# Kernel optimization log

Hardware: AMD Instinct MI355X
Metric: run time of the kernel (lower is better)

Reference implementation:

```python
import jax, jax.numpy as jnp
import numpy as np

WS = 7        # window_size
SHIFT = 3     # shift_size
NH = 3        # num_heads
E = 96        # embed_dim
B, H, W = 8, 224, 224


def _relative_position_index(ws: int) -> np.ndarray:
    coords = np.stack(np.meshgrid(np.arange(ws), np.arange(ws), indexing='ij')).reshape(2, -1)
    rel = coords[:, :, None] - coords[:, None, :]          # (2, N, N)
    rel = rel.transpose(1, 2, 0) + (ws - 1)                # (N, N, 2)
    rel[:, :, 0] *= 2 * ws - 1
    return rel.sum(-1)                                      # (N, N) in [0, (2ws-1)^2)


def setup_inputs() -> dict:
    key = jax.random.key(0)
    ks = jax.random.split(key, 6)
    x = jax.random.normal(ks[0], (B, H, W, E), dtype=jnp.float32)
    # nn.MultiheadAttention params: packed in_proj (3E,E)+(3E,), out_proj (E,E)+(E,)
    w_qkv = jax.random.normal(ks[1], (3 * E, E), dtype=jnp.float32) * 0.02
    b_qkv = jax.random.normal(ks[2], (3 * E,), dtype=jnp.float32) * 0.02
    w_out = jax.random.normal(ks[3], (E, E), dtype=jnp.float32) * 0.02
    b_out = jax.random.normal(ks[4], (E,), dtype=jnp.float32) * 0.02
    bias_table = jax.random.normal(ks[5], ((2 * WS - 1) ** 2, NH), dtype=jnp.float32) * 0.02
    rel_index = jnp.asarray(_relative_position_index(WS), dtype=jnp.int32)
    return {"x": x, "w_qkv": w_qkv, "b_qkv": b_qkv, "w_out": w_out,
            "b_out": b_out, "bias_table": bias_table, "rel_index": rel_index}


def reference(x, w_qkv, b_qkv, w_out, b_out, bias_table, rel_index):
    ws, shift = WS, SHIFT
    Bq, Hq, Wq, C = x.shape
    nh = bias_table.shape[-1]
    hd = C // nh
    N = ws * ws

    # cyclic shift
    xs = jnp.roll(x, (-shift, -shift), axis=(1, 2))

    Hp = -(-Hq // ws) * ws
    Wp = -(-Wq // ws) * ws
    xs = jnp.pad(xs, ((0, 0), (0, Hp - Hq), (0, Wp - Wq), (0, 0)))

    # window partition -> (B*nW, N, C)
    win = xs.reshape(Bq, Hp // ws, ws, Wp // ws, ws, C)
    win = win.transpose(0, 1, 3, 2, 4, 5).reshape(-1, N, C)

    # packed QKV projection (torch Linear: x @ W.T + b)
    qkv = win @ w_qkv.T + b_qkv
    q, k, v = jnp.split(qkv, 3, axis=-1)
    hsplit = lambda t: t.reshape(t.shape[0], N, nh, hd)
    q, k, v = hsplit(q), hsplit(k), hsplit(v)

    # scaled attention scores + relative position bias (used as attn_mask in torch)
    scale = 1.0 / jnp.sqrt(jnp.asarray(hd, dtype=q.dtype))
    scores = jnp.einsum('bnhd,bmhd->bhnm', q * scale, k)    # (B*nW, h, N, N)
    bias = bias_table[rel_index].transpose(2, 0, 1)         # (h, N, N)
    attn = jax.nn.softmax(scores + bias[None], axis=-1)

    out = jnp.einsum('bhnm,bmhd->bnhd', attn, v).reshape(-1, N, C)
    out = out @ w_out.T + b_out

    # window reverse + crop + reverse shift
    out = out.reshape(Bq, Hp // ws, Wp // ws, ws, ws, C)
    out = out.transpose(0, 1, 3, 2, 4, 5).reshape(Bq, Hp, Wp, C)[:, :Hq, :Wq, :]
    return jnp.roll(out, (shift, shift), axis=(1, 2))
```

## Files before the change

### kernel.cpp

```cpp
#include <hip/hip_runtime.h>
#include <cstddef>


typedef _Float16 half8 __attribute__((ext_vector_type(8)));
typedef float f4v __attribute__((ext_vector_type(4)));
typedef unsigned short u16;
typedef unsigned int u32;

#define MFMA(A, B, C) __builtin_amdgcn_mfma_f32_16x16x32_f16((A), (B), (C), 0, 0, 0)

__device__ inline u16 f16b(float f) { return __builtin_bit_cast(u16, (_Float16)f); }
__device__ inline u32 pkrtz(float a, float b) {
    return __builtin_bit_cast(u32, __builtin_amdgcn_cvt_pkrtz(a, b));
}
__device__ inline int SWU(int a, int kg) {
    return (((a ^ (kg << 1) ^ ((a & 8) >> 1)) & 15) | (kg << 4));
}

__global__ void prep_kernel(const float* __restrict__ wqkv, const float* __restrict__ wout,
                            const float* __restrict__ btab, const int* __restrict__ ridx,
                            const float* __restrict__ bqkv,
                            u16* __restrict__ wq16, u16* __restrict__ wo16,
                            float* __restrict__ bmat, float* __restrict__ bqs)
{
    const int i = blockIdx.x * 256 + threadIdx.x;
    const float QS = 0.17677669529663688f * 1.4426950408889634f;
    if (i < 27648) {
        float f = wqkv[i];
        if (i < 9216) f *= QS;
        wq16[i] = f16b(f);
    } else if (i < 36864) {
        wo16[i - 27648] = f16b(wout[i - 27648]);
    } else if (i < 49152) {
        const int j = i - 36864;
        const int h = j >> 12, rem = j & 4095, r = rem >> 6, u = rem & 63;
        bmat[j] = (r < 49 && u < 49) ? btab[ridx[r * 49 + u] * 3 + h] * 1.4426950408889634f : 0.f;
    } else if (i < 49440) {
        const int j = i - 49152;
        float f = bqkv[j];
        if (j < 96) f *= QS;
        bqs[j] = f;
    }
}

__global__ __launch_bounds__(256, 4)
void swin_kernel(const float* __restrict__ x,
                 const u16* __restrict__ wq16,
                 const u16* __restrict__ wo16,
                 const float* __restrict__ bqs,
                 const float* __restrict__ bout,
                 const float* __restrict__ bm,
                 float* __restrict__ out)
{
    __shared__ __attribute__((aligned(16))) char smem[40960];
    constexpr int QT = 0, KT = 12288, VT = 24576, PL = 36864;

    const int tid  = threadIdx.x;
    const int w    = tid >> 6;
    const int lane = tid & 63;
    const int l15  = lane & 15;
    const int lg   = lane >> 4;

    const int blk = blockIdx.x;
    const int bb  = blk >> 10;
    const int wi7 = ((blk >> 5) & 31) * 7;
    const int wj7 = (blk & 31) * 7;

    const int swbase = SWU(l15, lg) * 16;
    const int elb    = ((lg & 1) * 4) * 2;

    half8 xb[4][3];
    #pragma unroll
    for (int m = 0; m < 4; ++m) {
        const int t = m * 16 + l15;
        const int tr = t / 7, tc = t - tr * 7;
        int r = wi7 + tr + 3; if (r >= 224) r -= 224;
        int c = wj7 + tc + 3; if (c >= 224) c -= 224;
        const float* xrow = x + ((size_t)((bb * 224 + r) * 224 + c)) * 96 + lg * 8;
        #pragma unroll
        for (int ks = 0; ks < 3; ++ks) {
            const float4 f0 = *(const float4*)(xrow + ks * 32);
            const float4 f1 = *(const float4*)(xrow + ks * 32 + 4);
            uint4 pk;
            pk.x = pkrtz(f0.x, f0.y); pk.y = pkrtz(f0.z, f0.w);
            pk.z = pkrtz(f1.x, f1.y); pk.w = pkrtz(f1.z, f1.w);
            xb[m][ks] = __builtin_bit_cast(half8, pk);
        }
    }
    {
        const u16* wbase = wq16 + (size_t)l15 * 96 + lg * 8;
        half8 bcur[3], bnxt[3];
        int n = w;
        {
            const u16* p = wbase + n * 1536;
            bcur[0] = *(const half8*)(p);
            bcur[1] = *(const half8*)(p + 32);
            bcur[2] = *(const half8*)(p + 64);
        }
        while (true) {
            const int n2 = n + 4;
            if (n2 < 18) {
                const u16* p = wbase + n2 * 1536;
                bnxt[0] = *(const half8*)(p);
                bnxt[1] = *(const half8*)(p + 32);
                bnxt[2] = *(const half8*)(p + 64);
            }
            if (n < 12) {
                const float4 b4 = *(const float4*)(bqs + n * 16 + lg * 4);
                const int kg = ((n & 1) << 1) + (lg >> 1);
                const int fr0 = (n < 6) ? (QT + (((n >> 1) * 4) << 10))
                                        : (KT + ((((n - 6) >> 1) * 4) << 10));
                #pragma unroll
                for (int m = 0; m < 4; ++m) {
                    f4v acc = {0.f, 0.f, 0.f, 0.f};
                    acc = MFMA(bcur[0], xb[m][0], acc);
                    acc = MFMA(bcur[1], xb[m][1], acc);
                    acc = MFMA(bcur[2], xb[m][2], acc);
                    uint2 pv;
                    pv.x = pkrtz(acc[0] + b4.x, acc[1] + b4.y);
                    pv.y = pkrtz(acc[2] + b4.z, acc[3] + b4.w);
                    *(uint2*)(smem + fr0 + (m << 10) + SWU(l15, kg) * 16 + elb) = pv;
                }
            } else {
                const float bv = bqs[n * 16 + l15];
                const int hh = (n - 12) >> 1, nd = n & 1;
                const int fr0 = VT + (((hh * 2 + nd) * 2) << 10);
                #pragma unroll
                for (int m = 0; m < 4; ++m) {
                    f4v acc = {0.f, 0.f, 0.f, 0.f};
                    acc = MFMA(xb[m][0], bcur[0], acc);
                    acc = MFMA(xb[m][1], bcur[1], acc);
                    acc = MFMA(xb[m][2], bcur[2], acc);
                    uint2 pv;
                    pv.x = pkrtz(acc[0] + bv, acc[1] + bv);
                    pv.y = pkrtz(acc[2] + bv, acc[3] + bv);
                    const int kg = ((m & 1) << 1) + (lg >> 1);
                    *(uint2*)(smem + fr0 + ((m >> 1) << 10) + SWU(l15, kg) * 16 + elb) = pv;
                }
            }
            if (n2 >= 18) break;
            bcur[0] = bnxt[0]; bcur[1] = bnxt[1]; bcur[2] = bnxt[2];
            n = n2;
        }
    }
    __syncthreads();

    {
        const int t = w * 16 + l15;
        half8 qa = *(const half8*)(smem + QT + ((0 * 4 + w) << 10) + swbase);
        half8 kb[4];
        #pragma unroll
        for (int ut = 0; ut < 4; ++ut)
            kb[ut] = *(const half8*)(smem + KT + ((0 * 4 + ut) << 10) + swbase);

        #pragma unroll
        for (int h = 0; h < 3; ++h) {
            const int qfr = QT + ((h * 4 + w) << 10);
            f4v s[4];
            #pragma unroll
            for (int ut = 0; ut < 4; ++ut) {
                f4v z = {0.f, 0.f, 0.f, 0.f};
                s[ut] = MFMA(kb[ut], qa, z);
            }
            half8 qan; half8 kbn[4];
            if (h < 2) {
                qan = *(const half8*)(smem + QT + (((h + 1) * 4 + w) << 10) + swbase);
                #pragma unroll
                for (int ut = 0; ut < 4; ++ut)
                    kbn[ut] = *(const half8*)(smem + KT + (((h + 1) * 4 + ut) << 10) + swbase);
            }
            const float* bp = bm + h * 4096 + t * 64 + lg * 4;
            #pragma unroll
            for (int ut = 0; ut < 4; ++ut) {
                const float4 bv = *(const float4*)(bp + ut * 16);
                s[ut][0] += bv.x; s[ut][1] += bv.y; s[ut][2] += bv.z; s[ut][3] += bv.w;
            }
            s[3][1] = -1e30f; s[3][2] = -1e30f; s[3][3] = -1e30f;
            if (lg) s[3][0] = -1e30f;
            float mx = -1e30f;
            #pragma unroll
            for (int ut = 0; ut < 4; ++ut)
                #pragma unroll
                for (int i = 0; i < 4; ++i) mx = fmaxf(mx, s[ut][i]);
            mx = fmaxf(mx, __shfl_xor(mx, 16));
            mx = fmaxf(mx, __shfl_xor(mx, 32));
            float sm = 0.f;
            #pragma unroll
            for (int ut = 0; ut < 4; ++ut)
                #pragma unroll
                for (int i = 0; i < 4; ++i) {
                    const float e = exp2f(s[ut][i] - mx);
                    s[ut][i] = e; sm += e;
                }
            sm += __shfl_xor(sm, 16);
            sm += __shfl_xor(sm, 32);
            const float inv = 1.f / sm;
            #pragma unroll
            for (int ut = 0; ut < 4; ++ut) {
                uint2 pv;
                pv.x = pkrtz(s[ut][0] * inv, s[ut][1] * inv);
                pv.y = pkrtz(s[ut][2] * inv, s[ut][3] * inv);
                const int kg = (ut & 1) * 2 + (lg >> 1);
                const int base = (ut < 2) ? qfr : (PL + (w << 10));
                *(uint2*)(smem + base + SWU(l15, kg) * 16 + elb) = pv;
            }
            const half8 p0 = *(const half8*)(smem + qfr + swbase);
            const half8 p1 = *(const half8*)(smem + PL + (w << 10) + swbase);
            #pragma unroll
            for (int nd = 0; nd < 2; ++nd) {
                f4v o = {0.f, 0.f, 0.f, 0.f};
                o = MFMA(*(const half8*)(smem + VT + (((h * 2 + nd) * 2 + 0) << 10) + swbase), p0, o);
                o = MFMA(*(const half8*)(smem + VT + (((h * 2 + nd) * 2 + 1) << 10) + swbase), p1, o);
                uint2 ov;
                ov.x = pkrtz(o[0], o[1]);
                ov.y = pkrtz(o[2], o[3]);
                const int kg = nd * 2 + (lg >> 1);
                *(uint2*)(smem + qfr + SWU(l15, kg) * 16 + elb) = ov;
            }
            if (h < 2) {
                qa = qan;
                #pragma unroll
                for (int ut = 0; ut < 4; ++ut) kb[ut] = kbn[ut];
            }
        }
    }
    __syncthreads();

    {
        #pragma unroll
        for (int q = 0; q < 6; ++q) {
            const int p = w * 6 + q;
            const int nn = p >> 2, m = p & 3;
            f4v acc = {0.f, 0.f, 0.f, 0.f};
            #pragma unroll
            for (int ks = 0; ks < 3; ++ks) {
                const half8 wa = *(const half8*)(wo16 + (size_t)(nn * 16 + l15) * 96 + ks * 32 + lg * 8);
                const half8 ob = *(const half8*)(smem + QT + ((ks * 4 + m) << 10) + swbase);
                acc = MFMA(wa, ob, acc);
            }
            const int t = m * 16 + l15;
            if (t < 49) {
                const int tr = t / 7, tc = t - tr * 7;
                int r = wi7 + tr + 3; if (r >= 224) r -= 224;
                int c = wj7 + tc + 3; if (c >= 224) c -= 224;
                const float4 bo = *(const float4*)(bout + nn * 16 + lg * 4);
                float4 res;
                res.x = acc[0] + bo.x; res.y = acc[1] + bo.y;
                res.z = acc[2] + bo.z; res.w = acc[3] + bo.w;
                *(float4*)(out + ((size_t)((bb * 224 + r) * 224 + c)) * 96 + nn * 16 + lg * 4) = res;
            }
        }
    }
}

extern "C" void kernel_launch(void* const* d_in, const int* in_sizes, int n_in,
                              void* d_out, int out_size, void* d_ws, size_t ws_size,
                              hipStream_t stream) {
    const float* x          = (const float*)d_in[0];
    const float* w_qkv      = (const float*)d_in[1];
    const float* b_qkv      = (const float*)d_in[2];
    const float* w_out      = (const float*)d_in[3];
    const float* b_out      = (const float*)d_in[4];
    const float* bias_table = (const float*)d_in[5];
    const int*   rel_index  = (const int*)d_in[6];
    float* outp = (float*)d_out;

    u16* wq16 = (u16*)d_ws;
    u16* wo16 = wq16 + 27648;
    float* bmat = (float*)((char*)d_ws + 73728);
    float* bqs  = (float*)((char*)d_ws + 122880);

    prep_kernel<<<dim3(194), dim3(256), 0, stream>>>(
        w_qkv, w_out, bias_table, rel_index, b_qkv, wq16, wo16, bmat, bqs);
    swin_kernel<<<dim3(8192), dim3(256), 0, stream>>>(
        x, wq16, wo16, bqs, b_out, bmat, outp);
}
```

Before: 219.2 us.

## Pre-fragment bias with mask, software-pipeline heads, drop barrier before out-projection

The bias matrix is now stored in MFMA fragment order with -inf padding baked in, so it can seed the score MFMA accumulator directly. This removes the per-head bias add and the masking writes. The score MFMAs for the next head are issued during the current head's softmax and PV stage, which overlaps the MFMA and VALU work. The out-projection is remapped so each wave uses only its own query rows from shared memory, which lets the final __syncthreads be dropped; the cost is more live registers for the double-buffered scores.

```diff
diff --git a/kernel.cpp b/kernel.cpp
--- a/kernel.cpp
+++ b/kernel.cpp
@@ -21,10 +21,11 @@
                             const float* __restrict__ btab, const int* __restrict__ ridx,
                             const float* __restrict__ bqkv,
                             u16* __restrict__ wq16, u16* __restrict__ wo16,
-                            float* __restrict__ bmat, float* __restrict__ bqs)
+                            float* __restrict__ bmf, float* __restrict__ bqs)
 {
     const int i = blockIdx.x * 256 + threadIdx.x;
-    const float QS = 0.17677669529663688f * 1.4426950408889634f;
+    const float LOG2E = 1.4426950408889634f;
+    const float QS = 0.17677669529663688f * LOG2E;
     if (i < 27648) {
         float f = wqkv[i];
         if (i < 9216) f *= QS;
@@ -32,9 +33,16 @@
     } else if (i < 36864) {
         wo16[i - 27648] = f16b(wout[i - 27648]);
     } else if (i < 49152) {
-        const int j = i - 36864;
-        const int h = j >> 12, rem = j & 4095, r = rem >> 6, u = rem & 63;
-        bmat[j] = (r < 49 && u < 49) ? btab[ridx[r * 49 + u] * 3 + h] * 1.4426950408889634f : 0.f;
+        const int j  = i - 36864;
+        const int fi = j & 3, ln = (j >> 2) & 63, fw = (j >> 8) & 3;
+        const int fut = (j >> 10) & 3, fh = j >> 12;
+        const int u  = fut * 16 + (ln >> 4) * 4 + fi;
+        const int tt = fw * 16 + (ln & 15);
+        float v;
+        if (u >= 49)      v = -1e30f;
+        else if (tt >= 49) v = 0.f;
+        else               v = btab[ridx[tt * 49 + u] * 3 + fh] * LOG2E;
+        bmf[j] = v;
     } else if (i < 49440) {
         const int j = i - 49152;
         float f = bqkv[j];
@@ -49,7 +57,7 @@
                  const u16* __restrict__ wo16,
                  const float* __restrict__ bqs,
                  const float* __restrict__ bout,
-                 const float* __restrict__ bm,
+                 const float* __restrict__ bmf,
                  float* __restrict__ out)
 {
     __shared__ __attribute__((aligned(16))) char smem[40960];
@@ -146,42 +154,44 @@
     __syncthreads();
 
     {
-        const int t = w * 16 + l15;
-        half8 qa = *(const half8*)(smem + QT + ((0 * 4 + w) << 10) + swbase);
-        half8 kb[4];
+        const int plb = PL + (w << 10);
+        half8 qaC, qaN;
+        half8 kb[2][4];
+        f4v   s[2][4];
+        f4v   bC[4];
+
+        qaC = *(const half8*)(smem + QT + ((0 * 4 + w) << 10) + swbase);
         #pragma unroll
         for (int ut = 0; ut < 4; ++ut)
-            kb[ut] = *(const half8*)(smem + KT + ((0 * 4 + ut) << 10) + swbase);
+            kb[0][ut] = *(const half8*)(smem + KT + ((0 * 4 + ut) << 10) + swbase);
+        {
+            const float* bb0 = bmf + w * 256 + lane * 4;
+            #pragma unroll
+            for (int ut = 0; ut < 4; ++ut) bC[ut] = *(const f4v*)(bb0 + ut * 1024);
+        }
+        #pragma unroll
+        for (int ut = 0; ut < 4; ++ut)
+            s[0][ut] = MFMA(kb[0][ut], qaC, bC[ut]);
 
         #pragma unroll
         for (int h = 0; h < 3; ++h) {
+            const int cur = h & 1, nxt = cur ^ 1;
             const int qfr = QT + ((h * 4 + w) << 10);
-            f4v s[4];
-            #pragma unroll
-            for (int ut = 0; ut < 4; ++ut) {
-                f4v z = {0.f, 0.f, 0.f, 0.f};
-                s[ut] = MFMA(kb[ut], qa, z);
-            }
-            half8 qan; half8 kbn[4];
             if (h < 2) {
-                qan = *(const half8*)(smem + QT + (((h + 1) * 4 + w) << 10) + swbase);
+                qaN = *(const half8*)(smem + QT + (((h + 1) * 4 + w) << 10) + swbase);
                 #pragma unroll
                 for (int ut = 0; ut < 4; ++ut)
-                    kbn[ut] = *(const half8*)(smem + KT + (((h + 1) * 4 + ut) << 10) + swbase);
-            }
-            const float* bp = bm + h * 4096 + t * 64 + lg * 4;
-            #pragma unroll
-            for (int ut = 0; ut < 4; ++ut) {
-                const float4 bv = *(const float4*)(bp + ut * 16);
-                s[ut][0] += bv.x; s[ut][1] += bv.y; s[ut][2] += bv.z; s[ut][3] += bv.w;
-            }
-            s[3][1] = -1e30f; s[3][2] = -1e30f; s[3][3] = -1e30f;
-            if (lg) s[3][0] = -1e30f;
-            float mx = -1e30f;
-            #pragma unroll
-            for (int ut = 0; ut < 4; ++ut)
-                #pragma unroll
-                for (int i = 0; i < 4; ++i) mx = fmaxf(mx, s[ut][i]);
+                    kb[nxt][ut] = *(const half8*)(smem + KT + (((h + 1) * 4 + ut) << 10) + swbase);
+                const float* bbn = bmf + (h + 1) * 4096 + w * 256 + lane * 4;
+                #pragma unroll
+                for (int ut = 0; ut < 4; ++ut) bC[ut] = *(const f4v*)(bbn + ut * 1024);
+            }
+            float mx = fmaxf(fmaxf(s[cur][0][0], s[cur][0][1]), fmaxf(s[cur][0][2], s[cur][0][3]));
+            #pragma unroll
+            for (int ut = 1; ut < 4; ++ut) {
+                mx = fmaxf(mx, fmaxf(fmaxf(s[cur][ut][0], s[cur][ut][1]),
+                                     fmaxf(s[cur][ut][2], s[cur][ut][3])));
+            }
             mx = fmaxf(mx, __shfl_xor(mx, 16));
             mx = fmaxf(mx, __shfl_xor(mx, 32));
             float sm = 0.f;
@@ -189,8 +199,8 @@
             for (int ut = 0; ut < 4; ++ut)
                 #pragma unroll
                 for (int i = 0; i < 4; ++i) {
-                    const float e = exp2f(s[ut][i] - mx);
-                    s[ut][i] = e; sm += e;
+                    const float e = exp2f(s[cur][ut][i] - mx);
+                    s[cur][ut][i] = e; sm += e;
                 }
             sm += __shfl_xor(sm, 16);
             sm += __shfl_xor(sm, 32);
@@ -198,56 +208,61 @@
             #pragma unroll
             for (int ut = 0; ut < 4; ++ut) {
                 uint2 pv;
-                pv.x = pkrtz(s[ut][0] * inv, s[ut][1] * inv);
-                pv.y = pkrtz(s[ut][2] * inv, s[ut][3] * inv);
+                pv.x = pkrtz(s[cur][ut][0] * inv, s[cur][ut][1] * inv);
+                pv.y = pkrtz(s[cur][ut][2] * inv, s[cur][ut][3] * inv);
                 const int kg = (ut & 1) * 2 + (lg >> 1);
-                const int base = (ut < 2) ? qfr : (PL + (w << 10));
+                const int base = (ut < 2) ? qfr : plb;
                 *(uint2*)(smem + base + SWU(l15, kg) * 16 + elb) = pv;
             }
+            const half8 vb00 = *(const half8*)(smem + VT + (((h * 2 + 0) * 2 + 0) << 10) + swbase);
+            const half8 vb01 = *(const half8*)(smem + VT + (((h * 2 + 0) * 2 + 1) << 10) + swbase);
+            const half8 vb10 = *(const half8*)(smem + VT + (((h * 2 + 1) * 2 + 0) << 10) + swbase);
+            const half8 vb11 = *(const half8*)(smem + VT + (((h * 2 + 1) * 2 + 1) << 10) + swbase);
+            if (h < 2) {
+                #pragma unroll
+                for (int ut = 0; ut < 4; ++ut)
+                    s[nxt][ut] = MFMA(kb[nxt][ut], qaN, bC[ut]);
+            }
             const half8 p0 = *(const half8*)(smem + qfr + swbase);
-            const half8 p1 = *(const half8*)(smem + PL + (w << 10) + swbase);
+            const half8 p1 = *(const half8*)(smem + plb + swbase);
             #pragma unroll
             for (int nd = 0; nd < 2; ++nd) {
                 f4v o = {0.f, 0.f, 0.f, 0.f};
-                o = MFMA(*(const half8*)(smem + VT + (((h * 2 + nd) * 2 + 0) << 10) + swbase), p0, o);
-                o = MFMA(*(const half8*)(smem + VT + (((h * 2 + nd) * 2 + 1) << 10) + swbase), p1, o);
+                o = MFMA(nd ? vb10 : vb00, p0, o);
+                o = MFMA(nd ? vb11 : vb01, p1, o);
                 uint2 ov;
                 ov.x = pkrtz(o[0], o[1]);
                 ov.y = pkrtz(o[2], o[3]);
-                const int kg = nd * 2 + (lg >> 1);
-                *(uint2*)(smem + qfr + SWU(l15, kg) * 16 + elb) = ov;
-            }
-            if (h < 2) {
-                qa = qan;
-                #pragma unroll
-                for (int ut = 0; ut < 4; ++ut) kb[ut] = kbn[ut];
-            }
-        }
-    }
-    __syncthreads();
+                *(uint2*)(smem + qfr + SWU(l15, nd * 2 + (lg >> 1)) * 16 + elb) = ov;
+            }
+        }
+    }
 
     {
-        #pragma unroll
-        for (int q = 0; q < 6; ++q) {
-            const int p = w * 6 + q;
-            const int nn = p >> 2, m = p & 3;
+        const half8 ob0 = *(const half8*)(smem + QT + ((0 * 4 + w) << 10) + swbase);
+        const half8 ob1 = *(const half8*)(smem + QT + ((1 * 4 + w) << 10) + swbase);
+        const half8 ob2 = *(const half8*)(smem + QT + ((2 * 4 + w) << 10) + swbase);
+        const int t = w * 16 + l15;
+        float* obase = nullptr;
+        if (t < 49) {
+            const int tr = t / 7, tc = t - tr * 7;
+            int r = wi7 + tr + 3; if (r >= 224) r -= 224;
+            int c = wj7 + tc + 3; if (c >= 224) c -= 224;
+            obase = out + ((size_t)((bb * 224 + r) * 224 + c)) * 96;
+        }
+        #pragma unroll
+        for (int nn = 0; nn < 6; ++nn) {
+            const u16* wp = wo16 + (size_t)(nn * 16 + l15) * 96 + lg * 8;
             f4v acc = {0.f, 0.f, 0.f, 0.f};
-            #pragma unroll
-            for (int ks = 0; ks < 3; ++ks) {
-                const half8 wa = *(const half8*)(wo16 + (size_t)(nn * 16 + l15) * 96 + ks * 32 + lg * 8);
-                const half8 ob = *(const half8*)(smem + QT + ((ks * 4 + m) << 10) + swbase);
-                acc = MFMA(wa, ob, acc);
-            }
-            const int t = m * 16 + l15;
-            if (t < 49) {
-                const int tr = t / 7, tc = t - tr * 7;
-                int r = wi7 + tr + 3; if (r >= 224) r -= 224;
-                int c = wj7 + tc + 3; if (c >= 224) c -= 224;
+            acc = MFMA(*(const half8*)(wp),      ob0, acc);
+            acc = MFMA(*(const half8*)(wp + 32), ob1, acc);
+            acc = MFMA(*(const half8*)(wp + 64), ob2, acc);
+            if (obase) {
                 const float4 bo = *(const float4*)(bout + nn * 16 + lg * 4);
                 float4 res;
                 res.x = acc[0] + bo.x; res.y = acc[1] + bo.y;
                 res.z = acc[2] + bo.z; res.w = acc[3] + bo.w;
-                *(float4*)(out + ((size_t)((bb * 224 + r) * 224 + c)) * 96 + nn * 16 + lg * 4) = res;
+                *(float4*)(obase + nn * 16 + lg * 4) = res;
             }
         }
     }
@@ -267,11 +282,11 @@
 
     u16* wq16 = (u16*)d_ws;
     u16* wo16 = wq16 + 27648;
-    float* bmat = (float*)((char*)d_ws + 73728);
-    float* bqs  = (float*)((char*)d_ws + 122880);
+    float* bmf = (float*)((char*)d_ws + 73728);
+    float* bqs = (float*)((char*)d_ws + 122880);
 
     prep_kernel<<<dim3(194), dim3(256), 0, stream>>>(
-        w_qkv, w_out, bias_table, rel_index, b_qkv, wq16, wo16, bmat, bqs);
+        w_qkv, w_out, bias_table, rel_index, b_qkv, wq16, wo16, bmf, bqs);
     swin_kernel<<<dim3(8192), dim3(256), 0, stream>>>(
-        x, wq16, wo16, bqs, b_out, bmat, outp);
-}
+        x, wq16, wo16, bqs, b_out, bmf, outp);
+}
```

Result: faster. 208.7 us (-4.8%).
